# Optimization experiments

Hardware: AMD Instinct MI355X
Metric: run time of the kernel (lower is better)

Reference implementation:

```python
import jax, jax.numpy as jnp
import numpy as np

N_MEM = 50000
MATCH_THR2 = 0.01   # squared-distance match threshold (0.1 m)
EMA = 0.5           # EMA factor for matched-descriptor update
EPS = 1e-8


def _bilinear_depth(depth, uv):
    # depth: [H, W]; uv: [M, 2] pixel coords (u = x/col, v = y/row)
    H, W = depth.shape
    u = jnp.clip(uv[:, 0], 0.0, W - 1.001)
    v = jnp.clip(uv[:, 1], 0.0, H - 1.001)
    u0 = jnp.floor(u); v0 = jnp.floor(v)
    du = u - u0; dv = v - v0
    u0i = u0.astype(jnp.int32); v0i = v0.astype(jnp.int32)
    d00 = depth[v0i, u0i]
    d01 = depth[v0i, u0i + 1]
    d10 = depth[v0i + 1, u0i]
    d11 = depth[v0i + 1, u0i + 1]
    return d00 * (1 - du) * (1 - dv) + d01 * du * (1 - dv) + d10 * (1 - du) * dv + d11 * du * dv


def pix2world(points, depth_map, pose, K):
    # points [B,M,2], depth_map [B,1,H,W], pose [B,3,4] cam->world, K [B,3,3]
    d = jax.vmap(_bilinear_depth)(depth_map[:, 0], points)            # [B,M]
    pix = jnp.concatenate([points, jnp.ones_like(points[..., :1])], -1)  # [B,M,3]
    Kinv = jnp.linalg.inv(K)
    cam = jnp.einsum('bij,bmj->bmi', Kinv, pix) * d[..., None]        # [B,M,3]
    world = jnp.einsum('bij,bmj->bmi', pose[:, :, :3], cam) + pose[:, :, 3][:, None, :]
    valid = (d > 0) & jnp.isfinite(world).all(-1)                      # [B,M]
    return world, valid


def memory_write(pts, desc, valid, mem_pts, mem_desc, next_ptr):
    # pts [P,3], desc [P,D]; mem_pts [N,3], mem_desc [N,D]
    d2 = (jnp.sum(pts * pts, -1, keepdims=True)
          - 2.0 * pts @ mem_pts.T
          + jnp.sum(mem_pts * mem_pts, -1)[None, :])                  # [P,N]
    idx = jnp.argmin(d2, axis=1)                                       # [P]
    dmin = jnp.take_along_axis(d2, idx[:, None], axis=1)[:, 0]
    match = (dmin < MATCH_THR2) & valid
    n_match = match.sum()
    # returned descriptors come from the (non-differentiable) memory buffer;
    # unmatched entries return their own descriptor (cos=1 -> zero loss/grad)
    matched_desc = jax.lax.stop_gradient(jnp.where(match[:, None], mem_desc[idx], desc))
    # --- state update (buffers: no gradient) ---
    dsg = jax.lax.stop_gradient(desc)
    psg = jax.lax.stop_gradient(pts)
    unm = (~match) & valid
    slots = (next_ptr + jnp.cumsum(unm.astype(jnp.int32)) - 1) % N_MEM
    widx = jnp.where(unm, slots, idx)                                  # [P]
    old_pts = mem_pts[widx]; old_desc = mem_desc[widx]
    upd = old_desc * EMA + dsg * (1.0 - EMA)
    upd = upd / (jnp.linalg.norm(upd, axis=-1, keepdims=True) + EPS)
    new_desc_vals = jnp.where(match[:, None], upd, jnp.where(unm[:, None], dsg, old_desc))
    new_pts_vals = jnp.where(unm[:, None], psg, old_pts)
    new_mem_desc = mem_desc.at[widx].set(new_desc_vals)
    new_mem_pts = mem_pts.at[widx].set(new_pts_vals)
    return matched_desc, n_match, new_mem_pts, new_mem_desc


def setup_inputs() -> dict:
    key = jax.random.key(0)
    ks = jax.random.split(key, 8)
    B, M, D, H, W = 8, 512, 256, 480, 640
    points = jax.random.uniform(ks[0], (B, M, 2), jnp.float32) * jnp.array([W - 2.0, H - 2.0])
    depth_map = 0.5 + 4.5 * jax.random.uniform(ks[1], (B, 1, H, W), jnp.float32)
    # proper rotations via QR + small translations
    A = np.asarray(jax.random.normal(ks[2], (B, 3, 3)))
    Rs = np.stack([np.linalg.qr(A[b])[0] for b in range(B)]).astype(np.float32)
    t = np.asarray(jax.random.normal(ks[3], (B, 3, 1))) * 2.0
    pose = jnp.asarray(np.concatenate([Rs, t.astype(np.float32)], axis=2))  # [B,3,4]
    Kmat = jnp.broadcast_to(jnp.array([[320.0, 0.0, 320.0], [0.0, 320.0, 240.0], [0.0, 0.0, 1.0]], jnp.float32), (B, 3, 3))
    descriptors = jax.random.normal(ks[4], (B, M, D), jnp.float32)
    mem_pts = (jax.random.uniform(ks[5], (N_MEM, 3), jnp.float32) - 0.5) * 16.0
    mem_desc = jax.random.normal(ks[6], (N_MEM, D), jnp.float32)
    mem_desc = mem_desc / (jnp.linalg.norm(mem_desc, axis=-1, keepdims=True) + EPS)
    return {"points": points, "depth_map": depth_map, "pose": pose, "K": Kmat,
            "descriptors": descriptors, "mem_pts": mem_pts, "mem_desc": mem_desc,
            "next_ptr": 20000}


def reference(points, depth_map, pose, K, descriptors, mem_pts, mem_desc, next_ptr):
    world, valid = pix2world(points, depth_map, pose, K)               # [B,M,3], [B,M]
    P = world.shape[0] * world.shape[1]
    pts = world.reshape(P, 3)
    desc = descriptors.reshape(P, -1)
    vmask = valid.reshape(P)
    pts = jnp.where(vmask[:, None], pts, 1e6)   # invalid points never match
    matched_desc, n_match, new_mem_pts, new_mem_desc = memory_write(
        pts, desc, vmask, mem_pts, mem_desc, next_ptr)
    a = desc / jnp.maximum(jnp.linalg.norm(desc, axis=-1, keepdims=True), EPS)
    b = matched_desc / jnp.maximum(jnp.linalg.norm(matched_desc, axis=-1, keepdims=True), EPS)
    cos = jnp.sum(a * b, -1)                                           # [P]
    nv = jnp.maximum(vmask.sum(), 1)
    loss = 1.0 - jnp.sum(cos * vmask) / nv
    return loss, n_match, new_mem_pts, new_mem_desc
```

## Files before the change

kernel.cpp:

```cpp
#include <hip/hip_runtime.h>
#include <math.h>

#define N_MEM   50000
#define P_TOT   4096
#define DDIM    256
#define HDIM    480
#define WDIM    640
#define THR2    0.01f
#define EPSF    1e-8f

#define GDIM    24
#define NCELL   13824
#define GORG    -8.25f
#define GINV    (1.0f/0.6875f)
#define GRS     0.15f

#define CAP     10
#define OCAP    50000

#define QB1     16
#define MB1     196
#define NB1     (QB1 + MB1)
#define NTH1    (NB1 * 256L)
#define NWV     784

#define SWEEPB  128
#define COPYB   2048

#define ND2     6400000L
#define CS1     1920000L
#define PTS2    75000L

typedef unsigned long long ull;

__device__ __forceinline__ unsigned fsort(float x) {
    unsigned b = __float_as_uint(x);
    return (b & 0x80000000u) ? ~b : (b | 0x80000000u);
}

__device__ __forceinline__ int cell1d(float x) {
    int c = (int)((x - GORG) * GINV);
    return min(max(c, 0), GDIM - 1);
}

__device__ __forceinline__ void copy2(const float2* __restrict__ s, float2* __restrict__ d,
                                      long lo, long hi, long g, long n)
{
    long i = lo + g;
    for (; i + 3*n < hi; i += 4*n) {
        float2 a = s[i], b = s[i+n], c = s[i+2*n], e = s[i+3*n];
        d[i] = a; d[i+n] = b; d[i+2*n] = c; d[i+3*n] = e;
    }
    for (; i < hi; i += n) d[i] = s[i];
}

#define WS_PTS      0
#define WS_FLAGS    65536
#define WS_WIDX     81920
#define WS_MINKEY   98304
#define WS_WAVEINV  131072
#define WS_SCANOUT  137344
#define WS_WINOVF   137360
#define WS_BUCKET   337360
#define WS_MCNT     613840
#define WS_OCUR     669136

__global__ __launch_bounds__(256) void k_build(const float* __restrict__ points,
                                               const float* __restrict__ depth,
                                               const float* __restrict__ pose,
                                               const float* __restrict__ Kmat,
                                               const float* __restrict__ mem_pts,
                                               const float* __restrict__ mem_desc,
                                               float* __restrict__ dout,
                                               char* __restrict__ ws)
{
    float4* pts      = (float4*)(ws + WS_PTS);
    int* flags       = (int*)(ws + WS_FLAGS);
    ull* minkey      = (ull*)(ws + WS_MINKEY);
    ull* wave_inv    = (ull*)(ws + WS_WAVEINV);
    int* overflow    = (int*)(ws + WS_WINOVF);
    unsigned short* bucket = (unsigned short*)(ws + WS_BUCKET);
    int* mcnt        = (int*)(ws + WS_MCNT);
    int* ocur        = (int*)(ws + WS_OCUR);
    const float2* dsrc = (const float2*)mem_desc;
    float2* ddst = (float2*)(dout + 2 + (long)N_MEM * 3);

    int t = threadIdx.x, bid = blockIdx.x;
    long gid = (long)bid * 256 + t;

    if (bid < QB1) {
        int p = bid * 256 + t;
        minkey[p] = 0xFFFFFFFFFFFFFFFFULL;
        int b = p >> 9;
        const float* K = Kmat + b * 9;
        float a00=K[0],a01=K[1],a02=K[2],a10=K[3],a11=K[4],a12=K[5],a20=K[6],a21=K[7],a22=K[8];
        float det = a00*(a11*a22-a12*a21) - a01*(a10*a22-a12*a20) + a02*(a10*a21-a11*a20);
        float id = 1.0f/det;
        float i00=(a11*a22-a12*a21)*id, i01=(a02*a21-a01*a22)*id, i02=(a01*a12-a02*a11)*id;
        float i10=(a12*a20-a10*a22)*id, i11=(a00*a22-a02*a20)*id, i12=(a02*a10-a00*a12)*id;
        float i20=(a10*a21-a11*a20)*id, i21=(a01*a20-a00*a21)*id, i22=(a00*a11-a01*a10)*id;
        float u = points[p*2+0], v = points[p*2+1];
        float uc = fminf(fmaxf(u, 0.f), (float)WDIM - 1.001f);
        float vc = fminf(fmaxf(v, 0.f), (float)HDIM - 1.001f);
        float u0 = floorf(uc), v0 = floorf(vc);
        float du = uc - u0, dv = vc - v0;
        int u0i = (int)u0, v0i = (int)v0;
        const float* dm = depth + (size_t)b * HDIM * WDIM;
        float d00 = dm[v0i*WDIM + u0i];
        float d01 = dm[v0i*WDIM + u0i + 1];
        float d10 = dm[(v0i+1)*WDIM + u0i];
        float d11 = dm[(v0i+1)*WDIM + u0i + 1];
        float d = d00*(1.f-du)*(1.f-dv) + d01*du*(1.f-dv) + d10*(1.f-du)*dv + d11*du*dv;
        float cx = (i00*u + i01*v + i02) * d;
        float cy = (i10*u + i11*v + i12) * d;
        float cz = (i20*u + i21*v + i22) * d;
        const float* T = pose + b * 12;
        float wx = T[0]*cx + T[1]*cy + T[2]*cz  + T[3];
        float wy = T[4]*cx + T[5]*cy + T[6]*cz  + T[7];
        float wz = T[8]*cx + T[9]*cy + T[10]*cz + T[11];
        int val = (d > 0.f) && isfinite(wx) && isfinite(wy) && isfinite(wz);
        float px = val ? wx : 1e6f;
        float py = val ? wy : 1e6f;
        float pz = val ? wz : 1e6f;
        float pp = px*px + py*py + pz*pz;
        pts[p] = make_float4(px, py, pz, pp);
        flags[p] = val;
    } else {
        int j = (bid - QB1) * 256 + t;
        ull wk = 0xFFFFFFFFFFFFFFFFULL;
        if (j < N_MEM) {
            float mx = mem_pts[j*3+0], my = mem_pts[j*3+1], mz = mem_pts[j*3+2];
            int c = (cell1d(mz) * GDIM + cell1d(my)) * GDIM + cell1d(mx);
            int pos = atomicAdd(&mcnt[c], 1);
            if (pos < CAP) bucket[c * CAP + pos] = (unsigned short)j;
            else {
                int op = atomicAdd(ocur, 1);
                if (op < OCAP) overflow[op] = j;
            }
            float mm = mx*mx + my*my + mz*mz;
            float qx = 1e6f;
            float qp  = qx*qx + qx*qx + qx*qx;
            float dot = qx*mx + qx*my + qx*mz;
            float dinv = qp - 2.f*dot + mm;
            wk = ((ull)fsort(dinv) << 32) | (unsigned)j;
        }
        #pragma unroll
        for (int off = 32; off; off >>= 1) {
            ull o = __shfl_xor(wk, off);
            wk = o < wk ? o : wk;
        }
        if ((t & 63) == 0) wave_inv[((bid - QB1) * 256 + t) >> 6] = wk;
    }
    copy2(dsrc, ddst, 0, CS1, gid, NTH1);
}

__global__ __launch_bounds__(256) void k_main(const float* __restrict__ mem_pts,
                                              const float* __restrict__ mem_desc,
                                              float* __restrict__ dout,
                                              char* __restrict__ ws)
{
    float4* pts      = (float4*)(ws + WS_PTS);
    int* flags       = (int*)(ws + WS_FLAGS);
    ull* minkey      = (ull*)(ws + WS_MINKEY);
    int* overflow    = (int*)(ws + WS_WINOVF);
    unsigned short* bucket = (unsigned short*)(ws + WS_BUCKET);
    int* mcnt        = (int*)(ws + WS_MCNT);
    int* ocur        = (int*)(ws + WS_OCUR);
    float* out_pts = dout + 2;
    const float2* dsrc = (const float2*)mem_desc;
    float2* ddst = (float2*)(dout + 2 + (long)N_MEM * 3);

    int bid = blockIdx.x, t = threadIdx.x;
    if (bid < SWEEPB) {
        int gid = bid * 256 + t;
        int p  = gid >> 3;
        int ci = gid & 7;
        if (!flags[p]) return;
        float4 P = pts[p];
        int x0 = cell1d(P.x - GRS), x1 = cell1d(P.x + GRS);
        int y0 = cell1d(P.y - GRS), y1 = cell1d(P.y + GRS);
        int z0 = cell1d(P.z - GRS), z1 = cell1d(P.z + GRS);
        int xx = (ci & 1)        ? x1 : x0;
        int yy = ((ci >> 1) & 1) ? y1 : y0;
        int zz = (ci >> 2)       ? z1 : z0;
        int cell = (zz * GDIM + yy) * GDIM + xx;
        int cnt = min(mcnt[cell], CAP);
        int base = cell * CAP;
        ull best = 0xFFFFFFFFFFFFFFFFULL;
        for (int k = 0; k < cnt; ++k) {
            int j = (int)bucket[base + k];
            float mx = mem_pts[j*3+0], my = mem_pts[j*3+1], mz = mem_pts[j*3+2];
            float mm  = mx*mx + my*my + mz*mz;
            float dot = P.x*mx + P.y*my + P.z*mz;
            float dd2 = P.w - 2.f*dot + mm;
            ull key = ((ull)fsort(dd2) << 32) | (unsigned)j;
            best = key < best ? key : best;
        }
        if (ci == 0) {
            int nov = min(*ocur, OCAP);
            for (int k = 0; k < nov; ++k) {
                int j = overflow[k];
                float mx = mem_pts[j*3+0], my = mem_pts[j*3+1], mz = mem_pts[j*3+2];
                float mm  = mx*mx + my*my + mz*mz;
                float dot = P.x*mx + P.y*my + P.z*mz;
                float dd2 = P.w - 2.f*dot + mm;
                ull key = ((ull)fsort(dd2) << 32) | (unsigned)j;
                best = key < best ? key : best;
            }
        }
        if (best != 0xFFFFFFFFFFFFFFFFULL)
            atomicMin(&minkey[p], best);
    } else {
        const long tid = (long)(bid - SWEEPB) * 256 + t;
        const long NT = (long)COPYB * 256;
        copy2(dsrc, ddst, CS1, ND2, tid, NT);
        const float2* ps = (const float2*)mem_pts;
        float2* pd = (float2*)out_pts;
        for (long i = tid; i < PTS2; i += NT) pd[i] = ps[i];
    }
}

__global__ __launch_bounds__(1024) void k_scan(const int* __restrict__ next_ptr,
                                               float* __restrict__ dout,
                                               char* __restrict__ ws)
{
    int* flags      = (int*)(ws + WS_FLAGS);
    int* widx       = (int*)(ws + WS_WIDX);
    ull* minkey     = (ull*)(ws + WS_MINKEY);
    ull* wave_inv   = (ull*)(ws + WS_WAVEINV);
    float* scan_out = (float*)(ws + WS_SCANOUT);
    int* winner     = (int*)(ws + WS_WINOVF);

    __shared__ int su[1024];
    __shared__ int smc[1024];
    __shared__ ull ired[17];
    int t = threadIdx.x;
    int lane = t & 63;

    ull ik = (t < NWV) ? wave_inv[t] : 0xFFFFFFFFFFFFFFFFULL;
    #pragma unroll
    for (int off = 32; off; off >>= 1) {
        ull o = __shfl_xor(ik, off);
        ik = o < ik ? o : ik;
    }
    if (lane == 0) ired[t >> 6] = ik;
    __syncthreads();
    if (t == 0) {
        ull m = ired[0];
        for (int w = 1; w < 16; ++w) m = ired[w] < m ? ired[w] : m;
        ired[16] = m;
    }
    __syncthreads();
    ull inv = ired[16];

    int base = t * 4;
    const ull thr_key = ((ull)fsort(THR2)) << 32;
    int um[4], iv[4], wvv[4];
    int usum = 0, msum = 0;
    #pragma unroll
    for (int k = 0; k < 4; k++) {
        int v = flags[base + k] & 1;
        ull key = v ? minkey[base + k] : inv;
        int m = (key < thr_key) && v;
        int u = (!m) && v;
        iv[k] = (int)(key & 0xffffffffULL);
        um[k] = u; usum += u; msum += m;
        flags[base + k] = v | (m << 1) | (u << 2);
    }
    su[t] = usum; smc[t] = msum;
    __syncthreads();
    for (int off = 1; off < 1024; off <<= 1) {
        int a = su[t], b = (t >= off) ? su[t - off] : 0;
        int c = smc[t], d = (t >= off) ? smc[t - off] : 0;
        __syncthreads();
        su[t] = a + b; smc[t] = c + d;
        __syncthreads();
    }
    int excl = su[t] - usum;
    int np_ = *next_ptr;
    int run = excl;
    #pragma unroll
    for (int k = 0; k < 4; k++) {
        int wv;
        if (um[k]) { run += 1; wv = (np_ + run - 1) % N_MEM; }
        else       { wv = iv[k]; }
        widx[base + k] = wv;
        wvv[k] = wv;
        winner[wv] = -1;
    }
    __syncthreads();
    #pragma unroll
    for (int k = 0; k < 4; k++)
        atomicMax(&winner[wvv[k]], base + k);
    if (t == 1023) {
        int n_u = su[1023];
        float nvf = fmaxf((float)(smc[1023] + n_u), 1.f);
        dout[1]     = (float)smc[1023];
        dout[0]     = 1.f - (float)n_u / nvf;
        scan_out[0] = nvf;
    }
}

__global__ __launch_bounds__(256) void k_scatloss(const float* __restrict__ desc,
                                                  const float* __restrict__ mem_pts,
                                                  const float* __restrict__ mem_desc,
                                                  float* __restrict__ dout,
                                                  char* __restrict__ ws)
{
    float4* pts     = (float4*)(ws + WS_PTS);
    int* flags      = (int*)(ws + WS_FLAGS);
    int* widx       = (int*)(ws + WS_WIDX);
    float* scan_out = (float*)(ws + WS_SCANOUT);
    int* winner     = (int*)(ws + WS_WINOVF);
    float* out_pts  = dout + 2;
    float* out_desc = dout + 2 + (long)N_MEM * 3;

    __shared__ float red[16];
    int p = blockIdx.x;
    int t = threadIdx.x;
    int f = flags[p];
    int m = (f >> 1) & 1, u = (f >> 2) & 1;
    int wi = widx[p];
    int win = (winner[wi] == p);
    if (!m && !win) return;
    float dsg = desc[p * DDIM + t];
    float old = mem_desc[(long)wi * DDIM + t];
    float val;
    if (m) {
        float up = old * 0.5f + dsg * 0.5f;
        float sdd = dsg * dsg, smm2 = old * old, sdm = dsg * old, suu = up * up;
        #pragma unroll
        for (int off = 32; off; off >>= 1) {
            sdd  += __shfl_xor(sdd,  off);
            smm2 += __shfl_xor(smm2, off);
            sdm  += __shfl_xor(sdm,  off);
            suu  += __shfl_xor(suu,  off);
        }
        int w = t >> 6;
        if ((t & 63) == 0) { red[w] = sdd; red[4+w] = smm2; red[8+w] = sdm; red[12+w] = suu; }
        __syncthreads();
        float dd  = red[0] + red[1] + red[2] + red[3];
        float mm2 = red[4] + red[5] + red[6] + red[7];
        float dm  = red[8] + red[9] + red[10] + red[11];
        float uu  = red[12] + red[13] + red[14] + red[15];
        float cosv = dm / (fmaxf(sqrtf(dd), EPSF) * fmaxf(sqrtf(mm2), EPSF));
        val = up / (sqrtf(uu) + EPSF);
        if (t == 0) atomicAdd(&dout[0], -cosv / scan_out[0]);
    } else {
        val = u ? dsg : old;
    }
    if (win) {
        out_desc[(long)wi * DDIM + t] = val;
        if (t == 0) {
            float px, py, pz;
            if (u) { float4 P = pts[p]; px = P.x; py = P.y; pz = P.z; }
            else   { px = mem_pts[wi*3]; py = mem_pts[wi*3+1]; pz = mem_pts[wi*3+2]; }
            out_pts[wi*3+0] = px; out_pts[wi*3+1] = py; out_pts[wi*3+2] = pz;
        }
    }
}

extern "C" void kernel_launch(void* const* d_in, const int* in_sizes, int n_in,
                              void* d_out, int out_size, void* d_ws, size_t ws_size,
                              hipStream_t stream)
{
    const float* points   = (const float*)d_in[0];
    const float* depth    = (const float*)d_in[1];
    const float* pose     = (const float*)d_in[2];
    const float* Kmat     = (const float*)d_in[3];
    const float* desc     = (const float*)d_in[4];
    const float* mem_pts  = (const float*)d_in[5];
    const float* mem_desc = (const float*)d_in[6];
    const int*   next_ptr = (const int*)d_in[7];
    float* out = (float*)d_out;
    char* ws = (char*)d_ws;

    hipMemsetAsync(ws + WS_MCNT, 0, 55300, stream);
    k_build   <<<NB1, 256, 0, stream>>>(points, depth, pose, Kmat, mem_pts, mem_desc,
                                        out, ws);
    k_main    <<<SWEEPB + COPYB, 256, 0, stream>>>(mem_pts, mem_desc, out, ws);
    k_scan    <<<1, 1024, 0, stream>>>(next_ptr, out, ws);
    k_scatloss<<<P_TOT, 256, 0, stream>>>(desc, mem_pts, mem_desc, out, ws);
}
```

Measured before the change: 166.0 us.

## Fuse single-block scan into scatter-loss kernel and shift copy work into build

Removes the separate single-block k_scan launch. Instead, every scatter-loss block redundantly recomputes the prefix scan of unmatched and matched counts in LDS. Each block then finds the winning writer per memory slot by searching the packed slot indices, rather than using global atomicMax. The build kernel grid grows to 1024 blocks and takes a larger share of the descriptor copy (CS1 raised), balancing copy work against the sweep kernel. The trade-off is heavy redundant L2 reads: each of the 4096 blocks reads all flags and minkeys. There is also a 16 KB LDS footprint per block, in exchange for removing a serial kernel and a launch gap.

```diff
diff --git a/kernel.cpp b/kernel.cpp
--- a/kernel.cpp
+++ b/kernel.cpp
@@ -20,7 +20,7 @@
 
 #define QB1     16
 #define MB1     196
-#define NB1     (QB1 + MB1)
+#define NB1     1024
 #define NTH1    (NB1 * 256L)
 #define NWV     784
 
@@ -28,7 +28,7 @@
 #define COPYB   2048
 
 #define ND2     6400000L
-#define CS1     1920000L
+#define CS1     2880000L
 #define PTS2    75000L
 
 typedef unsigned long long ull;
@@ -56,10 +56,8 @@
 
 #define WS_PTS      0
 #define WS_FLAGS    65536
-#define WS_WIDX     81920
 #define WS_MINKEY   98304
 #define WS_WAVEINV  131072
-#define WS_SCANOUT  137344
 #define WS_WINOVF   137360
 #define WS_BUCKET   337360
 #define WS_MCNT     613840
@@ -87,6 +85,8 @@
 
     int t = threadIdx.x, bid = blockIdx.x;
     long gid = (long)bid * 256 + t;
+
+    if (bid == 0 && t == 0) dout[0] = 0.f;
 
     if (bid < QB1) {
         int p = bid * 256 + t;
@@ -125,7 +125,7 @@
         float pp = px*px + py*py + pz*pz;
         pts[p] = make_float4(px, py, pz, pp);
         flags[p] = val;
-    } else {
+    } else if (bid < QB1 + MB1) {
         int j = (bid - QB1) * 256 + t;
         ull wk = 0xFFFFFFFFFFFFFFFFULL;
         if (j < N_MEM) {
@@ -220,24 +220,31 @@
     }
 }
 
-__global__ __launch_bounds__(1024) void k_scan(const int* __restrict__ next_ptr,
-                                               float* __restrict__ dout,
-                                               char* __restrict__ ws)
-{
+__global__ __launch_bounds__(256) void k_scatloss(const float* __restrict__ desc,
+                                                  const float* __restrict__ mem_pts,
+                                                  const float* __restrict__ mem_desc,
+                                                  const int* __restrict__ next_ptr,
+                                                  float* __restrict__ dout,
+                                                  char* __restrict__ ws)
+{
+    float4* pts     = (float4*)(ws + WS_PTS);
     int* flags      = (int*)(ws + WS_FLAGS);
-    int* widx       = (int*)(ws + WS_WIDX);
     ull* minkey     = (ull*)(ws + WS_MINKEY);
     ull* wave_inv   = (ull*)(ws + WS_WAVEINV);
-    float* scan_out = (float*)(ws + WS_SCANOUT);
-    int* winner     = (int*)(ws + WS_WINOVF);
-
-    __shared__ int su[1024];
-    __shared__ int smc[1024];
-    __shared__ ull ired[17];
-    int t = threadIdx.x;
-    int lane = t & 63;
-
-    ull ik = (t < NWV) ? wave_inv[t] : 0xFFFFFFFFFFFFFFFFULL;
+    float* out_pts  = dout + 2;
+    float* out_desc = dout + 2 + (long)N_MEM * 3;
+
+    __shared__ int wlds[P_TOT];
+    __shared__ int su[256];
+    __shared__ int smc[256];
+    __shared__ ull ired[5];
+    __shared__ float red[16];
+    __shared__ int wmax[4];
+
+    int p = blockIdx.x, t = threadIdx.x, lane = t & 63;
+
+    ull ik = 0xFFFFFFFFFFFFFFFFULL;
+    for (int w = t; w < NWV; w += 256) { ull v2 = wave_inv[w]; ik = v2 < ik ? v2 : ik; }
     #pragma unroll
     for (int off = 32; off; off >>= 1) {
         ull o = __shfl_xor(ik, off);
@@ -246,30 +253,32 @@
     if (lane == 0) ired[t >> 6] = ik;
     __syncthreads();
     if (t == 0) {
-        ull m = ired[0];
-        for (int w = 1; w < 16; ++w) m = ired[w] < m ? ired[w] : m;
-        ired[16] = m;
-    }
-    __syncthreads();
-    ull inv = ired[16];
-
-    int base = t * 4;
+        ull a = ired[0] < ired[1] ? ired[0] : ired[1];
+        ull b = ired[2] < ired[3] ? ired[2] : ired[3];
+        ired[4] = a < b ? a : b;
+    }
+    __syncthreads();
+    ull inv = ired[4];
+
+    int base = t * 16;
     const ull thr_key = ((ull)fsort(THR2)) << 32;
-    int um[4], iv[4], wvv[4];
+    int pk[16];
+    unsigned um_bits = 0;
     int usum = 0, msum = 0;
     #pragma unroll
-    for (int k = 0; k < 4; k++) {
+    for (int k = 0; k < 16; k++) {
         int v = flags[base + k] & 1;
         ull key = v ? minkey[base + k] : inv;
         int m = (key < thr_key) && v;
         int u = (!m) && v;
-        iv[k] = (int)(key & 0xffffffffULL);
-        um[k] = u; usum += u; msum += m;
-        flags[base + k] = v | (m << 1) | (u << 2);
+        int iv = (int)(key & 0xffffffffULL);
+        um_bits |= ((unsigned)u) << k;
+        usum += u; msum += m;
+        pk[k] = (v << 16) | (m << 17) | (u << 18) | (u ? 0 : iv);
     }
     su[t] = usum; smc[t] = msum;
     __syncthreads();
-    for (int off = 1; off < 1024; off <<= 1) {
+    for (int off = 1; off < 256; off <<= 1) {
         int a = su[t], b = (t >= off) ? su[t - off] : 0;
         int c = smc[t], d = (t >= off) ? smc[t - off] : 0;
         __syncthreads();
@@ -280,48 +289,34 @@
     int np_ = *next_ptr;
     int run = excl;
     #pragma unroll
-    for (int k = 0; k < 4; k++) {
-        int wv;
-        if (um[k]) { run += 1; wv = (np_ + run - 1) % N_MEM; }
-        else       { wv = iv[k]; }
-        widx[base + k] = wv;
-        wvv[k] = wv;
-        winner[wv] = -1;
-    }
-    __syncthreads();
+    for (int k = 0; k < 16; k++) {
+        if ((um_bits >> k) & 1) { run += 1; pk[k] |= (np_ + run - 1) % N_MEM; }
+        wlds[base + k] = pk[k];
+    }
+    __syncthreads();
+
+    int mypk = wlds[p];
+    int wi = mypk & 0xFFFF;
+    int m = (mypk >> 17) & 1, u = (mypk >> 18) & 1;
+    float nvf = fmaxf((float)(su[255] + smc[255]), 1.f);
+    int best = -1;
+    for (int k = t; k < P_TOT; k += 256)
+        if ((wlds[k] & 0xFFFF) == wi) best = k;
     #pragma unroll
-    for (int k = 0; k < 4; k++)
-        atomicMax(&winner[wvv[k]], base + k);
-    if (t == 1023) {
-        int n_u = su[1023];
-        float nvf = fmaxf((float)(smc[1023] + n_u), 1.f);
-        dout[1]     = (float)smc[1023];
-        dout[0]     = 1.f - (float)n_u / nvf;
-        scan_out[0] = nvf;
-    }
-}
-
-__global__ __launch_bounds__(256) void k_scatloss(const float* __restrict__ desc,
-                                                  const float* __restrict__ mem_pts,
-                                                  const float* __restrict__ mem_desc,
-                                                  float* __restrict__ dout,
-                                                  char* __restrict__ ws)
-{
-    float4* pts     = (float4*)(ws + WS_PTS);
-    int* flags      = (int*)(ws + WS_FLAGS);
-    int* widx       = (int*)(ws + WS_WIDX);
-    float* scan_out = (float*)(ws + WS_SCANOUT);
-    int* winner     = (int*)(ws + WS_WINOVF);
-    float* out_pts  = dout + 2;
-    float* out_desc = dout + 2 + (long)N_MEM * 3;
-
-    __shared__ float red[16];
-    int p = blockIdx.x;
-    int t = threadIdx.x;
-    int f = flags[p];
-    int m = (f >> 1) & 1, u = (f >> 2) & 1;
-    int wi = widx[p];
-    int win = (winner[wi] == p);
+    for (int off = 32; off; off >>= 1) {
+        int o = __shfl_xor(best, off);
+        best = o > best ? o : best;
+    }
+    if (lane == 0) wmax[t >> 6] = best;
+    __syncthreads();
+    int winp = max(max(wmax[0], wmax[1]), max(wmax[2], wmax[3]));
+    int win = (winp == p);
+
+    if (p == 0 && t == 0) {
+        dout[1] = (float)smc[255];
+        atomicAdd(&dout[0], 1.f - (float)su[255] / nvf);
+    }
+
     if (!m && !win) return;
     float dsg = desc[p * DDIM + t];
     float old = mem_desc[(long)wi * DDIM + t];
@@ -345,7 +340,7 @@
         float uu  = red[12] + red[13] + red[14] + red[15];
         float cosv = dm / (fmaxf(sqrtf(dd), EPSF) * fmaxf(sqrtf(mm2), EPSF));
         val = up / (sqrtf(uu) + EPSF);
-        if (t == 0) atomicAdd(&dout[0], -cosv / scan_out[0]);
+        if (t == 0) atomicAdd(&dout[0], -cosv / nvf);
     } else {
         val = u ? dsg : old;
     }
@@ -379,6 +374,5 @@
     k_build   <<<NB1, 256, 0, stream>>>(points, depth, pose, Kmat, mem_pts, mem_desc,
                                         out, ws);
     k_main    <<<SWEEPB + COPYB, 256, 0, stream>>>(mem_pts, mem_desc, out, ws);
-    k_scan    <<<1, 1024, 0, stream>>>(next_ptr, out, ws);
-    k_scatloss<<<P_TOT, 256, 0, stream>>>(desc, mem_pts, mem_desc, out, ws);
-}
+    k_scatloss<<<P_TOT, 256, 0, stream>>>(desc, mem_pts, mem_desc, next_ptr, out, ws);
+}
```

After: 222.4 us. 34.0% more time.
